# Kernel optimization log

Measured on AMD Instinct MI355X. Metric: run time of the kernel, lower is better.

The kernel has to match this reference:

```python
import jax, jax.numpy as jnp
import numpy as np

COMMITMENT_COST = 0.25


def setup_inputs() -> dict:
    key = jax.random.key(0)
    k1, k2 = jax.random.split(key)
    inputs = jax.random.normal(k1, (32, 512, 32, 32), dtype=jnp.float32)
    embeddings = jax.random.normal(k2, (4096, 512), dtype=jnp.float32)
    return {"inputs": inputs, "embeddings": embeddings}


def reference(inputs, embeddings):
    # NCHW -> NHWC, flatten to (N, D)
    x = jnp.transpose(inputs, (0, 2, 3, 1))  # [B,H,W,D]
    D = embeddings.shape[1]
    z = x.reshape(-1, D)  # [N,D]

    # Squared L2 distances: ||z||^2 - 2 z E^T + ||E||^2
    d1 = jnp.sum(z * z, axis=1, keepdims=True)            # [N,1]
    d2 = 2.0 * jnp.matmul(z, embeddings.T)                # [N,K]
    d3 = jnp.sum(embeddings * embeddings, axis=1)[None]   # [1,K]
    distances = d1 - d2 + d3                              # [N,K]

    k = jnp.argmin(distances, axis=1)                     # [N]
    q = embeddings[k]                                     # [N,D] gather

    # latent loss: codebook loss + commitment loss
    e_loss = jnp.mean((jax.lax.stop_gradient(z) - q) ** 2)
    q_loss = COMMITMENT_COST * jnp.mean((z - jax.lax.stop_gradient(q)) ** 2)
    loss = e_loss + q_loss

    qx = q.reshape(x.shape)                               # [B,H,W,D]
    output = jnp.transpose(qx, (0, 3, 1, 2))              # NCHW
    return output, loss
```

## Files before the change

kernel.cpp:

```cpp
#include <hip/hip_runtime.h>

#define N_PTS 32768
#define DIM   512
#define KCODES 4096
#define HW    1024
#define MARGIN 0.125f
#define MAXFLAG 2048

typedef _Float16 half8 __attribute__((ext_vector_type(8)));
typedef float f32x4 __attribute__((ext_vector_type(4)));
typedef unsigned long long u64;

#define E16_OFF   0
#define BIAS_OFF  4194304
#define TOP2_OFF  4210688
#define ZC_OFF    5259264


__device__ __forceinline__ unsigned mono(float f) {
    unsigned u = __float_as_uint(f);
    return (u & 0x80000000u) ? ~u : (u | 0x80000000u);
}
__device__ __forceinline__ float unmono(unsigned m) {
    unsigned u = (m & 0x80000000u) ? (m & 0x7FFFFFFFu) : ~m;
    return __uint_as_float(u);
}

#define ASYNC16(src, dst) __builtin_amdgcn_global_load_lds( \
    (const __attribute__((address_space(1))) void*)(src), \
    (__attribute__((address_space(3))) void*)(dst), 16, 0, 0)

__global__ void prep_e_kernel(const float* __restrict__ E, _Float16* __restrict__ E16,
                              float* __restrict__ bias) {
    int k = blockIdx.x;
    int l = threadIdx.x;
    const float4* row = (const float4*)(E + (size_t)k * DIM);
    float4 a = row[l * 2];
    float4 b = row[l * 2 + 1];
    half8 h;
    h[0] = (_Float16)a.x; h[1] = (_Float16)a.y; h[2] = (_Float16)a.z; h[3] = (_Float16)a.w;
    h[4] = (_Float16)b.x; h[5] = (_Float16)b.y; h[6] = (_Float16)b.z; h[7] = (_Float16)b.w;
    *(half8*)(E16 + (size_t)k * DIM + l * 8) = h;
    float s = a.x * a.x + a.y * a.y + a.z * a.z + a.w * a.w +
              b.x * b.x + b.y * b.y + b.z * b.z + b.w * b.w;
#pragma unroll
    for (int off = 32; off > 0; off >>= 1) s += __shfl_down(s, off, 64);
    if (l == 0) bias[k] = 0.5f * s;
}

__global__ __launch_bounds__(256, 2) void score16_kernel(
    const float* __restrict__ in, const _Float16* __restrict__ E16,
    const float* __restrict__ bias, u64* __restrict__ top2)
{
    __shared__ alignas(16) _Float16 stage[4][1024 * 8];
    __shared__ alignas(16) float bias_sm[2048];

    const int t    = threadIdx.x;
    const int lane = t & 63;
    const int w    = t >> 6;
    const int lm   = lane & 15;
    const int lq   = lane >> 4;
    const int ks   = blockIdx.x;
    const int pt0  = blockIdx.y * 128;

    half8 zf[2][16];
#pragma unroll
    for (int pt = 0; pt < 2; pt++) {
        const int n = pt0 + 32 * w + 16 * pt + lm;
        const float* zb = in + (size_t)(n >> 10) * (DIM * HW) + (n & 1023);
#pragma unroll
        for (int kc = 0; kc < 16; kc++) {
            const int d0 = kc * 32 + lq * 8;
            half8 h;
#pragma unroll
            for (int j = 0; j < 8; j++) h[j] = (_Float16)zb[(size_t)(d0 + j) << 10];
            zf[pt][kc] = h;
        }
    }
    asm volatile("s_waitcnt vmcnt(0)" ::: "memory");

#pragma unroll
    for (int i = 0; i < 2; i++)
        ASYNC16(bias + ks * 2048 + (w * 2 + i) * 256 + lane * 4,
                &bias_sm[(w * 2 + i) * 256]);

    auto stage_half = [&](int b, int fn, int hn) {
        const int cn = ks * 2048 + (fn & 63) * 32;
#pragma unroll
        for (int i = 0; i < 4; i++) {
            const int kcp = 2 * w + (i >> 1);
            const int ct  = i & 1;
            ASYNC16(E16 + (size_t)(cn + ct * 16 + lm) * DIM + hn * 256 + kcp * 32 + lq * 8,
                    &stage[b][(size_t)(256 * w + 64 * i) << 3]);
        }
    };

    stage_half(0, 0, 0);
    stage_half(1, 0, 1);
    stage_half(2, 1, 0);

    const u64 PKNEG = ((u64)0x007FFFFFu) << 32;
    u64 b1[2], b2[2];
    float thr2[2];
#pragma unroll
    for (int p = 0; p < 2; p++) { b1[p] = PKNEG; b2[p] = PKNEG; thr2[p] = -INFINITY; }

    for (int f = 0; f < 64; f++) {
        const int code0 = ks * 2048 + f * 32;
        const int bA = (2 * f) & 3;
        const int bB = (2 * f + 1) & 3;

        f32x4 acc[2][2];

        asm volatile("s_waitcnt vmcnt(8)" ::: "memory");
        __builtin_amdgcn_s_barrier();
        asm volatile("" ::: "memory");
        stage_half((2 * f + 3) & 3, f + 1, 1);
#pragma unroll
        for (int ct = 0; ct < 2; ct++) {
            const float4 bv = *(const float4*)&bias_sm[f * 32 + ct * 16 + lq * 4];
            f32x4 bi; bi[0] = -bv.x; bi[1] = -bv.y; bi[2] = -bv.z; bi[3] = -bv.w;
            acc[ct][0] = bi; acc[ct][1] = bi;
        }
#pragma unroll
        for (int kc = 0; kc < 8; kc++) {
            half8 a0 = *(const half8*)&stage[bA][(size_t)(kc * 128 + lane) << 3];
            half8 a1 = *(const half8*)&stage[bA][(size_t)(kc * 128 + 64 + lane) << 3];
            acc[0][0] = __builtin_amdgcn_mfma_f32_16x16x32_f16(a0, zf[0][kc], acc[0][0], 0, 0, 0);
            acc[0][1] = __builtin_amdgcn_mfma_f32_16x16x32_f16(a0, zf[1][kc], acc[0][1], 0, 0, 0);
            acc[1][0] = __builtin_amdgcn_mfma_f32_16x16x32_f16(a1, zf[0][kc], acc[1][0], 0, 0, 0);
            acc[1][1] = __builtin_amdgcn_mfma_f32_16x16x32_f16(a1, zf[1][kc], acc[1][1], 0, 0, 0);
        }
        asm volatile("s_waitcnt lgkmcnt(0)" ::: "memory");

        asm volatile("s_waitcnt vmcnt(8)" ::: "memory");
        __builtin_amdgcn_s_barrier();
        asm volatile("" ::: "memory");
        stage_half((2 * f + 4) & 3, f + 2, 0);
#pragma unroll
        for (int kc = 0; kc < 8; kc++) {
            half8 a0 = *(const half8*)&stage[bB][(size_t)(kc * 128 + lane) << 3];
            half8 a1 = *(const half8*)&stage[bB][(size_t)(kc * 128 + 64 + lane) << 3];
            acc[0][0] = __builtin_amdgcn_mfma_f32_16x16x32_f16(a0, zf[0][8 + kc], acc[0][0], 0, 0, 0);
            acc[0][1] = __builtin_amdgcn_mfma_f32_16x16x32_f16(a0, zf[1][8 + kc], acc[0][1], 0, 0, 0);
            acc[1][0] = __builtin_amdgcn_mfma_f32_16x16x32_f16(a1, zf[0][8 + kc], acc[1][0], 0, 0, 0);
            acc[1][1] = __builtin_amdgcn_mfma_f32_16x16x32_f16(a1, zf[1][8 + kc], acc[1][1], 0, 0, 0);
        }
#pragma unroll
        for (int pt = 0; pt < 2; pt++) {
#pragma unroll
            for (int ct = 0; ct < 2; ct++) {
                f32x4 a = acc[ct][pt];
                bool hit = (a[0] > thr2[pt]) | (a[1] > thr2[pt]) |
                           (a[2] > thr2[pt]) | (a[3] > thr2[pt]);
                if (__any(hit)) {
#pragma unroll
                    for (int r = 0; r < 4; r++) {
                        float v = a[r];
                        if (v > thr2[pt]) {
                            int code = code0 + ct * 16 + lq * 4 + r;
                            u64 pk = ((u64)mono(v) << 32) | (unsigned)(0xFFFu ^ (unsigned)code);
                            if (pk > b1[pt]) { b2[pt] = b1[pt]; b1[pt] = pk; }
                            else if (pk > b2[pt]) { b2[pt] = pk; }
                            thr2[pt] = unmono((unsigned)(b2[pt] >> 32));
                        }
                    }
                }
            }
        }
        asm volatile("s_waitcnt lgkmcnt(0)" ::: "memory");
    }
    asm volatile("s_waitcnt vmcnt(0)" ::: "memory");

#pragma unroll
    for (int pt = 0; pt < 2; pt++) {
#pragma unroll
        for (int m = 16; m <= 32; m <<= 1) {
            u64 o1 = __shfl_xor(b1[pt], m, 64);
            u64 o2 = __shfl_xor(b2[pt], m, 64);
            u64 m1 = b1[pt] > o1 ? b1[pt] : o1;
            u64 lo = b1[pt] > o1 ? o1 : b1[pt];
            u64 mm = b2[pt] > o2 ? b2[pt] : o2;
            b2[pt] = lo > mm ? lo : mm;
            b1[pt] = m1;
        }
    }
    if (lq == 0) {
#pragma unroll
        for (int pt = 0; pt < 2; pt++) {
            const size_t p = (size_t)(pt0 + 32 * w + 16 * pt + lm);
            top2[p * 4 + ks * 2]     = b1[pt];
            top2[p * 4 + ks * 2 + 1] = b2[pt];
        }
    }
}

__global__ void merge_compact_kernel(const u64* __restrict__ top2, const float* __restrict__ in,
                                     int* __restrict__ k_final, int* __restrict__ list,
                                     int* __restrict__ count, float* __restrict__ zc) {
    int pt = blockIdx.x * 256 + threadIdx.x;
    const u64* p = top2 + (size_t)pt * 4;
    u64 B1 = 0, B2 = 0;
#pragma unroll
    for (int ks = 0; ks < 2; ks++) {
        u64 p1 = p[ks * 2], p2 = p[ks * 2 + 1];
        u64 m1 = B1 > p1 ? B1 : p1;
        u64 lo = B1 > p1 ? p1 : B1;
        u64 mm = B2 > p2 ? B2 : p2;
        B2 = lo > mm ? lo : mm;
        B1 = m1;
    }
    k_final[pt] = 0xFFF ^ (int)(B1 & 0xFFFull);
    float s1 = unmono((unsigned)(B1 >> 32));
    float s2 = unmono((unsigned)(B2 >> 32));
    if (s1 - s2 < MARGIN) {
        int idx = atomicAdd(count, 1);
        if (idx < MAXFLAG) {
            list[idx] = pt;
            const float* zb = in + (size_t)(pt >> 10) * (DIM * HW) + (pt & 1023);
            float* dst = zc + (size_t)idx * DIM;
#pragma unroll 8
            for (int d = 0; d < DIM; d++) dst[d] = zb[(size_t)d << 10];
        }
    }
}

__global__ __launch_bounds__(256) void rescore_kernel(
    const float* __restrict__ zc, const float* __restrict__ E,
    const float* __restrict__ bias, const int* __restrict__ count,
    u64* __restrict__ rb)
{
    __shared__ float As[16][128];
    __shared__ float Bs[16][132];

    int cnt = *count; if (cnt > MAXFLAG) cnt = MAXFLAG;
    const int t  = threadIdx.x;
    const int k0 = blockIdx.x * 128;
    const int r0 = blockIdx.y * 128;
    if (r0 >= cnt) return;

    float acc[8][8];
#pragma unroll
    for (int i = 0; i < 8; i++)
#pragma unroll
        for (int j = 0; j < 8; j++) acc[i][j] = 0.f;

    const int ra = (t >> 4) << 2;
    const int cb = (t & 15) << 2;

    for (int d0 = 0; d0 < DIM; d0 += 16) {
        {
            int j   = t >> 2;
            int dd4 = (t & 3) << 2;
            int rA = r0 + j;        if (rA >= cnt) rA = cnt - 1;
            int rB = r0 + j + 64;   if (rB >= cnt) rB = cnt - 1;
            float4 v0 = *(const float4*)&zc[(size_t)rA * DIM + d0 + dd4];
            float4 v1 = *(const float4*)&zc[(size_t)rB * DIM + d0 + dd4];
            As[dd4 + 0][j] = v0.x; As[dd4 + 1][j] = v0.y;
            As[dd4 + 2][j] = v0.z; As[dd4 + 3][j] = v0.w;
            As[dd4 + 0][j + 64] = v1.x; As[dd4 + 1][j + 64] = v1.y;
            As[dd4 + 2][j + 64] = v1.z; As[dd4 + 3][j + 64] = v1.w;
        }
        {
            int j   = t >> 2;
            int dd4 = (t & 3) << 2;
            const float* p = E + (size_t)(k0 + j) * DIM + d0 + dd4;
            float4 v0 = *(const float4*)p;
            float4 v1 = *(const float4*)(p + (size_t)64 * DIM);
            Bs[dd4 + 0][j] = v0.x; Bs[dd4 + 1][j] = v0.y;
            Bs[dd4 + 2][j] = v0.z; Bs[dd4 + 3][j] = v0.w;
            Bs[dd4 + 0][j + 64] = v1.x; Bs[dd4 + 1][j + 64] = v1.y;
            Bs[dd4 + 2][j + 64] = v1.z; Bs[dd4 + 3][j + 64] = v1.w;
        }
        __syncthreads();
#pragma unroll
        for (int dd = 0; dd < 16; dd++) {
            float4 a0 = *(const float4*)&As[dd][ra];
            float4 a1 = *(const float4*)&As[dd][ra + 64];
            float4 b0 = *(const float4*)&Bs[dd][cb];
            float4 b1v = *(const float4*)&Bs[dd][cb + 64];
            float av[8] = {a0.x, a0.y, a0.z, a0.w, a1.x, a1.y, a1.z, a1.w};
            float bv[8] = {b0.x, b0.y, b0.z, b0.w, b1v.x, b1v.y, b1v.z, b1v.w};
#pragma unroll
            for (int i = 0; i < 8; i++)
#pragma unroll
                for (int j = 0; j < 8; j++)
                    acc[i][j] = fmaf(av[i], bv[j], acc[i][j]);
        }
        __syncthreads();
    }

    float bcol[8];
#pragma unroll
    for (int j = 0; j < 8; j++) {
        int k = k0 + ((j < 4) ? (cb + j) : (64 + cb + j - 4));
        bcol[j] = bias[k];
    }
    u64 pk[8];
#pragma unroll
    for (int i = 0; i < 8; i++) {
        u64 bestp = 0ull;
#pragma unroll
        for (int j = 0; j < 8; j++) {
            int k = k0 + ((j < 4) ? (cb + j) : (64 + cb + j - 4));
            float s = acc[i][j] - bcol[j];
            u64 p = ((u64)mono(s) << 32) | (u64)(~(unsigned)k);
            if (p > bestp) bestp = p;
        }
        pk[i] = bestp;
    }
#pragma unroll
    for (int i = 0; i < 8; i++) {
#pragma unroll
        for (int off = 8; off > 0; off >>= 1) {
            u64 o = __shfl_down(pk[i], off, 16);
            if (o > pk[i]) pk[i] = o;
        }
    }
    if ((t & 15) == 0) {
#pragma unroll
        for (int i = 0; i < 8; i++) {
            int row = r0 + ((i < 4) ? (ra + i) : (64 + ra + i - 4));
            int slot = row < cnt ? row : cnt - 1;
            atomicMax(&rb[slot], pk[i]);
        }
    }
}

__global__ void apply_kernel(const int* __restrict__ list, const int* __restrict__ count,
                             const u64* __restrict__ rb, int* __restrict__ k_final) {
    int i = blockIdx.x * 256 + threadIdx.x;
    int cnt = *count; if (cnt > MAXFLAG) cnt = MAXFLAG;
    if (i < cnt) k_final[list[i]] = (int)(~(unsigned)(rb[i] & 0xffffffffull));
}

__global__ void gather_kernel(const float* __restrict__ in, const float* __restrict__ E,
                              const int* __restrict__ k_final,
                              float* __restrict__ out, float* __restrict__ sumsq)
{
    const int t  = threadIdx.x;
    const int tx = t & 63;
    const int ty = t >> 6;
    const int n  = blockIdx.x * 64 + tx;
    const int k  = k_final[n];
    const float* erow = E + (size_t)k * DIM;
    const size_t base = (size_t)(n >> 10) * (DIM * HW) + (n & 1023);
    float local = 0.f;
    for (int d = ty; d < DIM; d += 4) {
        float q = erow[d];
        size_t idx = base + ((size_t)d << 10);
        float z = in[idx];
        out[idx] = q;
        float df = z - q;
        local = fmaf(df, df, local);
    }
#pragma unroll
    for (int off = 32; off > 0; off >>= 1) local += __shfl_down(local, off, 64);
    __shared__ float red[4];
    if (tx == 0) red[ty] = local;
    __syncthreads();
    if (t == 0) atomicAdd(sumsq, red[0] + red[1] + red[2] + red[3]);
}

__global__ void finalize_kernel(const float* __restrict__ sumsq, float* __restrict__ out_loss) {
    *out_loss = 1.25f * (*sumsq) * (1.0f / 16777216.0f);
}

extern "C" void kernel_launch(void* const* d_in, const int* in_sizes, int n_in,
                              void* d_out, int out_size, void* d_ws, size_t ws_size,
                              hipStream_t stream) {
    const float* in = (const float*)d_in[0];
    const float* E  = (const float*)d_in[1];
    float* out = (float*)d_out;
    char* ob = (char*)d_out;

    _Float16* E16 = (_Float16*)(ob + E16_OFF);
    float* bias   = (float*)(ob + BIAS_OFF);
    u64* top2     = (u64*)(ob + TOP2_OFF);
    float* zc     = (float*)(ob + ZC_OFF);

    u64* rb      = (u64*)d_ws;
    int* count   = (int*)((char*)d_ws + 16384);
    float* sumsq = (float*)((char*)d_ws + 16388);
    int* list    = (int*)((char*)d_ws + 16392);
    int* k_final = (int*)((char*)d_ws + 24584);

    hipMemsetAsync(d_ws, 0, 16392, stream);

    prep_e_kernel<<<KCODES, 64, 0, stream>>>(E, E16, bias);

    score16_kernel<<<dim3(2, 256), 256, 0, stream>>>(in, E16, bias, top2);

    merge_compact_kernel<<<128, 256, 0, stream>>>(top2, in, k_final, list, count, zc);

    rescore_kernel<<<dim3(32, 16), 256, 0, stream>>>(zc, E, bias, count, rb);
    apply_kernel<<<8, 256, 0, stream>>>(list, count, rb, k_final);

    gather_kernel<<<N_PTS / 64, 256, 0, stream>>>(in, E, k_final, out, sumsq);
    finalize_kernel<<<1, 1, 0, stream>>>(sumsq, out + 16777216);
}
```

Before: 515.4 us.

## Enlarge score kernel block to 512 threads with 64-code tiles and triple buffering

The distance-scoring kernel now uses 8 waves per block covering 256 points, and each staged codebook chunk holds 64 codes instead of 32. Staging moves from four buffers to three, so each E16 tile in shared memory is reused by twice as many waves and per-wave accumulators double. The aim is to cut redundant codebook traffic and barriers per MFMA. In exchange, register pressure rises, LDS use per block grows, the prefetch depth shrinks, and the grid halves to 256 blocks, which may leave some CUs idle.

Result: no change. 512.8 us (-0.5%).

```diff
diff --git a/kernel.cpp b/kernel.cpp
--- a/kernel.cpp
+++ b/kernel.cpp
@@ -48,11 +48,11 @@
     if (l == 0) bias[k] = 0.5f * s;
 }
 
-__global__ __launch_bounds__(256, 2) void score16_kernel(
+__global__ __launch_bounds__(512, 2) void score16_kernel(
     const float* __restrict__ in, const _Float16* __restrict__ E16,
     const float* __restrict__ bias, u64* __restrict__ top2)
 {
-    __shared__ alignas(16) _Float16 stage[4][1024 * 8];
+    __shared__ alignas(16) _Float16 stage[3][16384];
     __shared__ alignas(16) float bias_sm[2048];
 
     const int t    = threadIdx.x;
@@ -61,7 +61,7 @@
     const int lm   = lane & 15;
     const int lq   = lane >> 4;
     const int ks   = blockIdx.x;
-    const int pt0  = blockIdx.y * 128;
+    const int pt0  = blockIdx.y * 256;
 
     half8 zf[2][16];
 #pragma unroll
@@ -79,25 +79,19 @@
     }
     asm volatile("s_waitcnt vmcnt(0)" ::: "memory");
 
-#pragma unroll
-    for (int i = 0; i < 2; i++)
-        ASYNC16(bias + ks * 2048 + (w * 2 + i) * 256 + lane * 4,
-                &bias_sm[(w * 2 + i) * 256]);
+    ASYNC16(bias + ks * 2048 + w * 256 + lane * 4, &bias_sm[w * 256]);
 
     auto stage_half = [&](int b, int fn, int hn) {
-        const int cn = ks * 2048 + (fn & 63) * 32;
+        const int cn = ks * 2048 + (fn & 31) * 64;
 #pragma unroll
         for (int i = 0; i < 4; i++) {
-            const int kcp = 2 * w + (i >> 1);
-            const int ct  = i & 1;
-            ASYNC16(E16 + (size_t)(cn + ct * 16 + lm) * DIM + hn * 256 + kcp * 32 + lq * 8,
-                    &stage[b][(size_t)(256 * w + 64 * i) << 3]);
+            ASYNC16(E16 + (size_t)(cn + i * 16 + lm) * DIM + hn * 256 + w * 32 + lq * 8,
+                    &stage[b][(size_t)(w * 4 + i) << 9]);
         }
     };
 
     stage_half(0, 0, 0);
     stage_half(1, 0, 1);
-    stage_half(2, 1, 0);
 
     const u64 PKNEG = ((u64)0x007FFFFFu) << 32;
     u64 b1[2], b2[2];
@@ -105,51 +99,51 @@
 #pragma unroll
     for (int p = 0; p < 2; p++) { b1[p] = PKNEG; b2[p] = PKNEG; thr2[p] = -INFINITY; }
 
-    for (int f = 0; f < 64; f++) {
-        const int code0 = ks * 2048 + f * 32;
-        const int bA = (2 * f) & 3;
-        const int bB = (2 * f + 1) & 3;
-
-        f32x4 acc[2][2];
-
-        asm volatile("s_waitcnt vmcnt(8)" ::: "memory");
+    for (int f = 0; f < 32; f++) {
+        const int code0 = ks * 2048 + f * 64;
+        const int bA = (2 * f) % 3;
+        const int bB = (2 * f + 1) % 3;
+
+        f32x4 acc[4][2];
+
+        asm volatile("s_waitcnt vmcnt(4)" ::: "memory");
         __builtin_amdgcn_s_barrier();
         asm volatile("" ::: "memory");
-        stage_half((2 * f + 3) & 3, f + 1, 1);
-#pragma unroll
-        for (int ct = 0; ct < 2; ct++) {
-            const float4 bv = *(const float4*)&bias_sm[f * 32 + ct * 16 + lq * 4];
+        stage_half((2 * f + 2) % 3, f + 1, 0);
+#pragma unroll
+        for (int ct = 0; ct < 4; ct++) {
+            const float4 bv = *(const float4*)&bias_sm[f * 64 + ct * 16 + lq * 4];
             f32x4 bi; bi[0] = -bv.x; bi[1] = -bv.y; bi[2] = -bv.z; bi[3] = -bv.w;
             acc[ct][0] = bi; acc[ct][1] = bi;
         }
 #pragma unroll
         for (int kc = 0; kc < 8; kc++) {
-            half8 a0 = *(const half8*)&stage[bA][(size_t)(kc * 128 + lane) << 3];
-            half8 a1 = *(const half8*)&stage[bA][(size_t)(kc * 128 + 64 + lane) << 3];
-            acc[0][0] = __builtin_amdgcn_mfma_f32_16x16x32_f16(a0, zf[0][kc], acc[0][0], 0, 0, 0);
-            acc[0][1] = __builtin_amdgcn_mfma_f32_16x16x32_f16(a0, zf[1][kc], acc[0][1], 0, 0, 0);
-            acc[1][0] = __builtin_amdgcn_mfma_f32_16x16x32_f16(a1, zf[0][kc], acc[1][0], 0, 0, 0);
-            acc[1][1] = __builtin_amdgcn_mfma_f32_16x16x32_f16(a1, zf[1][kc], acc[1][1], 0, 0, 0);
+#pragma unroll
+            for (int ct = 0; ct < 4; ct++) {
+                half8 a = *(const half8*)&stage[bA][(size_t)((kc * 4 + ct) * 512 + lane * 8)];
+                acc[ct][0] = __builtin_amdgcn_mfma_f32_16x16x32_f16(a, zf[0][kc], acc[ct][0], 0, 0, 0);
+                acc[ct][1] = __builtin_amdgcn_mfma_f32_16x16x32_f16(a, zf[1][kc], acc[ct][1], 0, 0, 0);
+            }
         }
         asm volatile("s_waitcnt lgkmcnt(0)" ::: "memory");
 
-        asm volatile("s_waitcnt vmcnt(8)" ::: "memory");
+        asm volatile("s_waitcnt vmcnt(4)" ::: "memory");
         __builtin_amdgcn_s_barrier();
         asm volatile("" ::: "memory");
-        stage_half((2 * f + 4) & 3, f + 2, 0);
+        stage_half((2 * f + 3) % 3, f + 1, 1);
 #pragma unroll
         for (int kc = 0; kc < 8; kc++) {
-            half8 a0 = *(const half8*)&stage[bB][(size_t)(kc * 128 + lane) << 3];
-            half8 a1 = *(const half8*)&stage[bB][(size_t)(kc * 128 + 64 + lane) << 3];
-            acc[0][0] = __builtin_amdgcn_mfma_f32_16x16x32_f16(a0, zf[0][8 + kc], acc[0][0], 0, 0, 0);
-            acc[0][1] = __builtin_amdgcn_mfma_f32_16x16x32_f16(a0, zf[1][8 + kc], acc[0][1], 0, 0, 0);
-            acc[1][0] = __builtin_amdgcn_mfma_f32_16x16x32_f16(a1, zf[0][8 + kc], acc[1][0], 0, 0, 0);
-            acc[1][1] = __builtin_amdgcn_mfma_f32_16x16x32_f16(a1, zf[1][8 + kc], acc[1][1], 0, 0, 0);
+#pragma unroll
+            for (int ct = 0; ct < 4; ct++) {
+                half8 a = *(const half8*)&stage[bB][(size_t)((kc * 4 + ct) * 512 + lane * 8)];
+                acc[ct][0] = __builtin_amdgcn_mfma_f32_16x16x32_f16(a, zf[0][8 + kc], acc[ct][0], 0, 0, 0);
+                acc[ct][1] = __builtin_amdgcn_mfma_f32_16x16x32_f16(a, zf[1][8 + kc], acc[ct][1], 0, 0, 0);
+            }
         }
 #pragma unroll
         for (int pt = 0; pt < 2; pt++) {
 #pragma unroll
-            for (int ct = 0; ct < 2; ct++) {
+            for (int ct = 0; ct < 4; ct++) {
                 f32x4 a = acc[ct][pt];
                 bool hit = (a[0] > thr2[pt]) | (a[1] > thr2[pt]) |
                            (a[2] > thr2[pt]) | (a[3] > thr2[pt]);
@@ -389,7 +383,7 @@
 
     prep_e_kernel<<<KCODES, 64, 0, stream>>>(E, E16, bias);
 
-    score16_kernel<<<dim3(2, 256), 256, 0, stream>>>(in, E16, bias, top2);
+    score16_kernel<<<dim3(2, 128), 512, 0, stream>>>(in, E16, bias, top2);
 
     merge_compact_kernel<<<128, 256, 0, stream>>>(top2, in, k_final, list, count, zc);
 
```
